# Kernel optimization log

Hardware: AMD Instinct MI355X
Metric: run time of the kernel (lower is better)

Reference implementation:

```python
import jax, jax.numpy as jnp
import numpy as np

E, T, D, H = 8, 2048, 1024, 4096
N_LAYER = 12

def setup_inputs() -> dict:
    key = jax.random.key(0)
    ks = jax.random.split(key, 4)
    x = jax.random.normal(ks[0], (E, T, D), dtype=jnp.float32)
    w_c_fc = jax.random.normal(ks[1], (E, D, H), dtype=jnp.float32) * 0.02
    w_gate = jax.random.normal(ks[2], (E, D, H), dtype=jnp.float32) * 0.02
    w_c_proj = jax.random.normal(ks[3], (E, H, D), dtype=jnp.float32) * (0.02 * (2 * N_LAYER) ** (-0.5))
    b_c_fc = jnp.zeros((E, 1, H), dtype=jnp.float32)
    b_gate = jnp.zeros((E, 1, H), dtype=jnp.float32)
    b_c_proj = jnp.zeros((E, 1, D), dtype=jnp.float32)
    return {"x": x, "w_c_fc": w_c_fc, "b_c_fc": b_c_fc, "w_gate": w_gate,
            "b_gate": b_gate, "w_c_proj": w_c_proj, "b_c_proj": b_c_proj}

def reference(x, w_c_fc, b_c_fc, w_gate, b_gate, w_c_proj, b_c_proj):
    # Per-expert SwiGLU FFN (grouped GEMM over expert dim e)
    h = jnp.einsum('eti,eih->eth', x, w_c_fc) + b_c_fc      # [E,T,H]
    g = jax.nn.silu(jnp.einsum('eti,eih->eth', x, w_gate) + b_gate)
    og = h * g                                               # gated hidden
    o = jnp.einsum('eth,eho->eto', og, w_c_proj) + b_c_proj  # [E,T,D]
    return o
```

## Files before the change

### kernel.cpp

```cpp
#include <hip/hip_runtime.h>

#define E 8
#define T 2048
#define D 1024
#define H 4096

using f32x4 = __attribute__((ext_vector_type(4))) float;
using frag8 = __attribute__((ext_vector_type(8))) short;

typedef unsigned int uint_as3 __attribute__((address_space(3)));
typedef unsigned int uint_as1 __attribute__((address_space(1)));

__device__ __forceinline__ unsigned short f2bf(float f) {
  unsigned int u = __float_as_uint(f);
  u += 0x7fffu + ((u >> 16) & 1u);
  return (unsigned short)(u >> 16);
}

__device__ __forceinline__ void gload16(const void* g, void* l) {
  __builtin_amdgcn_global_load_lds((const uint_as1*)g, (uint_as3*)l, 16, 0, 0);
}

__device__ __forceinline__ void stage8(const unsigned short* src, int ld,
                                       unsigned short* lds, int r0, int lane) {
  int lr = lane >> 3;
  int cs = lane & 7;
  int gc = cs ^ lr;
  const unsigned short* g = src + (size_t)(r0 + lr) * ld + gc * 8;
  unsigned short* l = lds + r0 * 64;
  gload16(g, l);
}

__device__ __forceinline__ frag8 read_frag(const unsigned short* lds, int row, int chunk) {
  return *(const frag8*)&lds[row * 64 + ((chunk ^ (row & 7)) << 3)];
}


__global__ __launch_bounds__(256) void convert_kernel(const float4* __restrict__ in,
                                                      ushort4* __restrict__ out, int n4) {
  int i = blockIdx.x * blockDim.x + threadIdx.x;
  int stride = gridDim.x * blockDim.x;
  for (; i < n4; i += stride) {
    float4 v = in[i];
    ushort4 o;
    o.x = f2bf(v.x); o.y = f2bf(v.y); o.z = f2bf(v.z); o.w = f2bf(v.w);
    out[i] = o;
  }
}

__global__ __launch_bounds__(256) void tconv_kernel(const float* __restrict__ in,
                                                    unsigned short* __restrict__ out,
                                                    int R, int C) {
  __shared__ float tile[32][33];
  int e = blockIdx.z;
  const float* src = in + (size_t)e * R * C;
  unsigned short* dst = out + (size_t)e * R * C;
  int c0 = blockIdx.x * 32, r0 = blockIdx.y * 32;
  int tx = threadIdx.x, ty = threadIdx.y;
#pragma unroll
  for (int i = 0; i < 32; i += 8)
    tile[ty + i][tx] = src[(size_t)(r0 + ty + i) * C + c0 + tx];
  __syncthreads();
#pragma unroll
  for (int i = 0; i < 32; i += 8)
    dst[(size_t)(c0 + ty + i) * R + r0 + tx] = f2bf(tile[tx][ty + i]);
}


__global__ __launch_bounds__(256) void gemm1_kernel(
    const unsigned short* __restrict__ xb,
    const unsigned short* __restrict__ wfcT,
    const unsigned short* __restrict__ wgT,
    const float* __restrict__ bfc,
    const float* __restrict__ bgate,
    unsigned short* __restrict__ og) {
  __shared__ unsigned short As[128 * 64];
  __shared__ unsigned short Bf[64 * 64];
  __shared__ unsigned short Bg[64 * 64];

  int bid = blockIdx.x;
  int e = bid >> 10;
  int mt = (bid >> 6) & 15;
  int nt = bid & 63;
  int m0 = mt * 128, n0 = nt * 64;

  int tid = threadIdx.x;
  int w = __builtin_amdgcn_readfirstlane(tid >> 6);
  int lane = tid & 63;

  const unsigned short* Abase = xb + (size_t)e * T * D + (size_t)m0 * D;
  const unsigned short* Fbase = wfcT + (size_t)e * H * D + (size_t)n0 * D;
  const unsigned short* Gbase = wgT + (size_t)e * H * D + (size_t)n0 * D;

  f32x4 acc_h[4][2] = {};
  f32x4 acc_g[4][2] = {};

  int wm = (w >> 1) * 64;
  int wn = (w & 1) * 32;
  int col = lane & 15, quad = lane >> 4;

  for (int k0 = 0; k0 < D; k0 += 64) {
#pragma unroll
    for (int j = 0; j < 4; ++j)
      stage8(Abase + k0, D, As, w * 32 + j * 8, lane);
#pragma unroll
    for (int j = 0; j < 2; ++j) {
      stage8(Fbase + k0, D, Bf, w * 16 + j * 8, lane);
      stage8(Gbase + k0, D, Bg, w * 16 + j * 8, lane);
    }
    __syncthreads();
#pragma unroll
    for (int kk = 0; kk < 64; kk += 32) {
      int chunk = (kk >> 3) + quad;
      frag8 a[4], fb[2], gb[2];
#pragma unroll
      for (int i = 0; i < 4; ++i)
        a[i] = read_frag(As, wm + i * 16 + col, chunk);
#pragma unroll
      for (int i = 0; i < 2; ++i) {
        fb[i] = read_frag(Bf, wn + i * 16 + col, chunk);
        gb[i] = read_frag(Bg, wn + i * 16 + col, chunk);
      }
#pragma unroll
      for (int mi = 0; mi < 4; ++mi)
#pragma unroll
        for (int ni = 0; ni < 2; ++ni) {
          acc_h[mi][ni] = __builtin_amdgcn_mfma_f32_16x16x32_bf16(a[mi], fb[ni], acc_h[mi][ni], 0, 0, 0);
          acc_g[mi][ni] = __builtin_amdgcn_mfma_f32_16x16x32_bf16(a[mi], gb[ni], acc_g[mi][ni], 0, 0, 0);
        }
    }
    __syncthreads();
  }

#pragma unroll
  for (int ni = 0; ni < 2; ++ni) {
    int n = n0 + wn + ni * 16 + col;
    float bh = bfc[e * H + n];
    float bg2 = bgate[e * H + n];
#pragma unroll
    for (int mi = 0; mi < 4; ++mi) {
#pragma unroll
      for (int i = 0; i < 4; ++i) {
        int m = m0 + wm + mi * 16 + quad * 4 + i;
        float hv = acc_h[mi][ni][i] + bh;
        float gv = acc_g[mi][ni][i] + bg2;
        float sg = gv / (1.0f + __expf(-gv));
        og[(size_t)e * T * H + (size_t)m * H + n] = f2bf(hv * sg);
      }
    }
  }
}


__global__ __launch_bounds__(256) void gemm2_kernel(
    const unsigned short* __restrict__ og,
    const unsigned short* __restrict__ wpT,
    const float* __restrict__ bproj,
    float* __restrict__ out) {
  __shared__ unsigned short As[128 * 64];
  __shared__ unsigned short Bs[128 * 64];

  int bid = blockIdx.x;
  int e = bid >> 7;
  int mt = (bid >> 3) & 15;
  int nt = bid & 7;
  int m0 = mt * 128, n0 = nt * 128;

  int tid = threadIdx.x;
  int w = __builtin_amdgcn_readfirstlane(tid >> 6);
  int lane = tid & 63;

  const unsigned short* Abase = og + (size_t)e * T * H + (size_t)m0 * H;
  const unsigned short* Bbase = wpT + (size_t)e * D * H + (size_t)n0 * H;

  f32x4 acc[4][4] = {};

  int wm = (w >> 1) * 64;
  int wn = (w & 1) * 64;
  int col = lane & 15, quad = lane >> 4;

  for (int k0 = 0; k0 < H; k0 += 64) {
#pragma unroll
    for (int j = 0; j < 4; ++j) {
      stage8(Abase + k0, H, As, w * 32 + j * 8, lane);
      stage8(Bbase + k0, H, Bs, w * 32 + j * 8, lane);
    }
    __syncthreads();
#pragma unroll
    for (int kk = 0; kk < 64; kk += 32) {
      int chunk = (kk >> 3) + quad;
      frag8 a[4], b[4];
#pragma unroll
      for (int i = 0; i < 4; ++i)
        a[i] = read_frag(As, wm + i * 16 + col, chunk);
#pragma unroll
      for (int i = 0; i < 4; ++i)
        b[i] = read_frag(Bs, wn + i * 16 + col, chunk);
#pragma unroll
      for (int mi = 0; mi < 4; ++mi)
#pragma unroll
        for (int ni = 0; ni < 4; ++ni)
          acc[mi][ni] = __builtin_amdgcn_mfma_f32_16x16x32_bf16(a[mi], b[ni], acc[mi][ni], 0, 0, 0);
    }
    __syncthreads();
  }

#pragma unroll
  for (int ni = 0; ni < 4; ++ni) {
    int n = n0 + wn + ni * 16 + col;
    float bb = bproj[e * D + n];
#pragma unroll
    for (int mi = 0; mi < 4; ++mi) {
#pragma unroll
      for (int i = 0; i < 4; ++i) {
        int m = m0 + wm + mi * 16 + quad * 4 + i;
        out[(size_t)e * T * D + (size_t)m * D + n] = acc[mi][ni][i] + bb;
      }
    }
  }
}


extern "C" void kernel_launch(void* const* d_in, const int* in_sizes, int n_in,
                              void* d_out, int out_size, void* d_ws, size_t ws_size,
                              hipStream_t stream) {
  const float* x = (const float*)d_in[0];
  const float* wfc = (const float*)d_in[1];
  const float* bfc = (const float*)d_in[2];
  const float* wg = (const float*)d_in[3];
  const float* bg = (const float*)d_in[4];
  const float* wp = (const float*)d_in[5];
  const float* bp = (const float*)d_in[6];
  float* out = (float*)d_out;

  char* ws = (char*)d_ws;
  unsigned short* xb = (unsigned short*)(ws);
  unsigned short* wfcT = (unsigned short*)(ws + 33554432);
  unsigned short* wgT = (unsigned short*)(ws + 100663296);
  unsigned short* wpT = (unsigned short*)(ws + 167772160);
  unsigned short* og = (unsigned short*)(ws + 234881024);

  convert_kernel<<<2048, 256, 0, stream>>>((const float4*)x, (ushort4*)xb,
                                           (int)((size_t)E * T * D / 4));
  tconv_kernel<<<dim3(H / 32, D / 32, E), dim3(32, 8), 0, stream>>>(wfc, wfcT, D, H);
  tconv_kernel<<<dim3(H / 32, D / 32, E), dim3(32, 8), 0, stream>>>(wg, wgT, D, H);
  tconv_kernel<<<dim3(D / 32, H / 32, E), dim3(32, 8), 0, stream>>>(wp, wpT, H, D);

  gemm1_kernel<<<E * (T / 128) * (H / 64), 256, 0, stream>>>(xb, wfcT, wgT, bfc, bg, og);
  gemm2_kernel<<<E * (T / 128) * (D / 128), 256, 0, stream>>>(og, wpT, bp, out);
}
```

Baseline: 1.038 ms.

## Triple-buffer LDS with async prefetch and larger 512-thread tiles in both GEMMs

Both GEMM kernels move to 512-thread blocks with larger output tiles (128x128 for gemm1, 256x128 for gemm2). The single-buffered load-sync-compute loop becomes a 3-stage LDS ring that prefetches tile t+2 via global_load_lds while computing tile t. Explicit vmcnt/lgkmcnt waits, raw s_barrier, sched_barrier and setprio interleave loads with MFMA bursts. The aim is to hide global memory latency and cut per-tile sync overhead, at the cost of more LDS per block (up to ~144KB in gemm1), lower occupancy, and fragile hand-counted waitcnts.

```diff
diff --git a/kernel.cpp b/kernel.cpp
--- a/kernel.cpp
+++ b/kernel.cpp
@@ -34,6 +34,9 @@
 __device__ __forceinline__ frag8 read_frag(const unsigned short* lds, int row, int chunk) {
   return *(const frag8*)&lds[row * 64 + ((chunk ^ (row & 7)) << 3)];
 }
+
+#define BARRIER() asm volatile("s_barrier" ::: "memory")
+#define WAIT_LGKM0() asm volatile("s_waitcnt lgkmcnt(0)" ::: "memory")
 
 
 __global__ __launch_bounds__(256) void convert_kernel(const float4* __restrict__ in,
@@ -67,69 +70,120 @@
 }
 
 
-__global__ __launch_bounds__(256) void gemm1_kernel(
+__global__ __launch_bounds__(512) void gemm1_kernel(
     const unsigned short* __restrict__ xb,
     const unsigned short* __restrict__ wfcT,
     const unsigned short* __restrict__ wgT,
     const float* __restrict__ bfc,
     const float* __restrict__ bgate,
     unsigned short* __restrict__ og) {
-  __shared__ unsigned short As[128 * 64];
-  __shared__ unsigned short Bf[64 * 64];
-  __shared__ unsigned short Bg[64 * 64];
+  __shared__ unsigned short As[3][128 * 64];
+  __shared__ unsigned short Bf[3][128 * 64];
+  __shared__ unsigned short Bg[3][128 * 64];
 
   int bid = blockIdx.x;
-  int e = bid >> 10;
-  int mt = (bid >> 6) & 15;
-  int nt = bid & 63;
-  int m0 = mt * 128, n0 = nt * 64;
+  int e = bid >> 9;
+  int mt = (bid >> 5) & 15;
+  int nt = bid & 31;
+  int m0 = mt * 128, n0 = nt * 128;
 
   int tid = threadIdx.x;
   int w = __builtin_amdgcn_readfirstlane(tid >> 6);
   int lane = tid & 63;
 
-  const unsigned short* Abase = xb + (size_t)e * T * D + (size_t)m0 * D;
-  const unsigned short* Fbase = wfcT + (size_t)e * H * D + (size_t)n0 * D;
-  const unsigned short* Gbase = wgT + (size_t)e * H * D + (size_t)n0 * D;
-
-  f32x4 acc_h[4][2] = {};
-  f32x4 acc_g[4][2] = {};
-
-  int wm = (w >> 1) * 64;
-  int wn = (w & 1) * 32;
+  const unsigned short* Ab = xb + (size_t)e * T * D + (size_t)m0 * D;
+  const unsigned short* Fb = wfcT + (size_t)e * H * D + (size_t)n0 * D;
+  const unsigned short* Gb = wgT + (size_t)e * H * D + (size_t)n0 * D;
+
+  f32x4 ah[4][2] = {};
+  f32x4 ag[4][2] = {};
+
+  int wm = (w >> 2) * 64;
+  int wn = (w & 3) * 32;
   int col = lane & 15, quad = lane >> 4;
-
-  for (int k0 = 0; k0 < D; k0 += 64) {
-#pragma unroll
-    for (int j = 0; j < 4; ++j)
-      stage8(Abase + k0, D, As, w * 32 + j * 8, lane);
-#pragma unroll
-    for (int j = 0; j < 2; ++j) {
-      stage8(Fbase + k0, D, Bf, w * 16 + j * 8, lane);
-      stage8(Gbase + k0, D, Bg, w * 16 + j * 8, lane);
-    }
-    __syncthreads();
-#pragma unroll
-    for (int kk = 0; kk < 64; kk += 32) {
-      int chunk = (kk >> 3) + quad;
-      frag8 a[4], fb[2], gb[2];
-#pragma unroll
-      for (int i = 0; i < 4; ++i)
-        a[i] = read_frag(As, wm + i * 16 + col, chunk);
-#pragma unroll
-      for (int i = 0; i < 2; ++i) {
-        fb[i] = read_frag(Bf, wn + i * 16 + col, chunk);
-        gb[i] = read_frag(Bg, wn + i * 16 + col, chunk);
+  int r0a = w * 8;
+
+  constexpr int NT = D / 64;
+
+#pragma unroll
+  for (int t0 = 0; t0 < 2; ++t0) {
+    stage8(Ab + t0 * 64, D, As[t0], r0a, lane);
+    stage8(Ab + t0 * 64, D, As[t0], r0a + 64, lane);
+    stage8(Fb + t0 * 64, D, Bf[t0], r0a, lane);
+    stage8(Fb + t0 * 64, D, Bf[t0], r0a + 64, lane);
+    stage8(Gb + t0 * 64, D, Bg[t0], r0a, lane);
+    stage8(Gb + t0 * 64, D, Bg[t0], r0a + 64, lane);
+  }
+  asm volatile("s_waitcnt vmcnt(6)" ::: "memory");
+  BARRIER();
+
+  int s = 0, s2 = 2;
+  for (int t = 0; t < NT; ++t) {
+    const unsigned short* Asl = As[s];
+    const unsigned short* Bfl = Bf[s];
+    const unsigned short* Bgl = Bg[s];
+    bool pf = (t + 2) < NT;
+    int kpre = (t + 2) * 64;
+
+    frag8 a[4], f[2], g[2];
+#pragma unroll
+    for (int i = 0; i < 4; ++i) a[i] = read_frag(Asl, wm + i * 16 + col, quad);
+#pragma unroll
+    for (int i = 0; i < 2; ++i) {
+      f[i] = read_frag(Bfl, wn + i * 16 + col, quad);
+      g[i] = read_frag(Bgl, wn + i * 16 + col, quad);
+    }
+    if (pf) {
+      stage8(Ab + kpre, D, As[s2], r0a, lane);
+      stage8(Ab + kpre, D, As[s2], r0a + 64, lane);
+      stage8(Fb + kpre, D, Bf[s2], r0a, lane);
+    }
+    BARRIER();
+    WAIT_LGKM0();
+    __builtin_amdgcn_sched_barrier(0);
+    __builtin_amdgcn_s_setprio(1);
+#pragma unroll
+    for (int mi = 0; mi < 4; ++mi)
+#pragma unroll
+      for (int ni = 0; ni < 2; ++ni) {
+        ah[mi][ni] = __builtin_amdgcn_mfma_f32_16x16x32_bf16(a[mi], f[ni], ah[mi][ni], 0, 0, 0);
+        ag[mi][ni] = __builtin_amdgcn_mfma_f32_16x16x32_bf16(a[mi], g[ni], ag[mi][ni], 0, 0, 0);
       }
-#pragma unroll
-      for (int mi = 0; mi < 4; ++mi)
-#pragma unroll
-        for (int ni = 0; ni < 2; ++ni) {
-          acc_h[mi][ni] = __builtin_amdgcn_mfma_f32_16x16x32_bf16(a[mi], fb[ni], acc_h[mi][ni], 0, 0, 0);
-          acc_g[mi][ni] = __builtin_amdgcn_mfma_f32_16x16x32_bf16(a[mi], gb[ni], acc_g[mi][ni], 0, 0, 0);
-        }
-    }
-    __syncthreads();
+    __builtin_amdgcn_s_setprio(0);
+    BARRIER();
+
+#pragma unroll
+    for (int i = 0; i < 4; ++i) a[i] = read_frag(Asl, wm + i * 16 + col, 4 + quad);
+#pragma unroll
+    for (int i = 0; i < 2; ++i) {
+      f[i] = read_frag(Bfl, wn + i * 16 + col, 4 + quad);
+      g[i] = read_frag(Bgl, wn + i * 16 + col, 4 + quad);
+    }
+    if (pf) {
+      stage8(Fb + kpre, D, Bf[s2], r0a + 64, lane);
+      stage8(Gb + kpre, D, Bg[s2], r0a, lane);
+      stage8(Gb + kpre, D, Bg[s2], r0a + 64, lane);
+    }
+    BARRIER();
+    WAIT_LGKM0();
+    __builtin_amdgcn_sched_barrier(0);
+    __builtin_amdgcn_s_setprio(1);
+#pragma unroll
+    for (int mi = 0; mi < 4; ++mi)
+#pragma unroll
+      for (int ni = 0; ni < 2; ++ni) {
+        ah[mi][ni] = __builtin_amdgcn_mfma_f32_16x16x32_bf16(a[mi], f[ni], ah[mi][ni], 0, 0, 0);
+        ag[mi][ni] = __builtin_amdgcn_mfma_f32_16x16x32_bf16(a[mi], g[ni], ag[mi][ni], 0, 0, 0);
+      }
+    __builtin_amdgcn_s_setprio(0);
+    if (pf)
+      asm volatile("s_waitcnt vmcnt(6)" ::: "memory");
+    else if (t + 2 == NT)
+      asm volatile("s_waitcnt vmcnt(0)" ::: "memory");
+    BARRIER();
+
+    s = (s == 2) ? 0 : s + 1;
+    s2 = (s2 == 2) ? 0 : s2 + 1;
   }
 
 #pragma unroll
@@ -142,8 +196,8 @@
 #pragma unroll
       for (int i = 0; i < 4; ++i) {
         int m = m0 + wm + mi * 16 + quad * 4 + i;
-        float hv = acc_h[mi][ni][i] + bh;
-        float gv = acc_g[mi][ni][i] + bg2;
+        float hv = ah[mi][ni][i] + bh;
+        float gv = ag[mi][ni][i] + bg2;
         float sg = gv / (1.0f + __expf(-gv));
         og[(size_t)e * T * H + (size_t)m * H + n] = f2bf(hv * sg);
       }
@@ -152,57 +206,104 @@
 }
 
 
-__global__ __launch_bounds__(256) void gemm2_kernel(
+__global__ __launch_bounds__(512) void gemm2_kernel(
     const unsigned short* __restrict__ og,
     const unsigned short* __restrict__ wpT,
     const float* __restrict__ bproj,
     float* __restrict__ out) {
-  __shared__ unsigned short As[128 * 64];
-  __shared__ unsigned short Bs[128 * 64];
+  __shared__ unsigned short As[3][256 * 64];
+  __shared__ unsigned short Bs[3][128 * 64];
 
   int bid = blockIdx.x;
-  int e = bid >> 7;
-  int mt = (bid >> 3) & 15;
+  int e = bid >> 6;
+  int mt = (bid >> 3) & 7;
   int nt = bid & 7;
-  int m0 = mt * 128, n0 = nt * 128;
+  int m0 = mt * 256, n0 = nt * 128;
 
   int tid = threadIdx.x;
   int w = __builtin_amdgcn_readfirstlane(tid >> 6);
   int lane = tid & 63;
 
-  const unsigned short* Abase = og + (size_t)e * T * H + (size_t)m0 * H;
-  const unsigned short* Bbase = wpT + (size_t)e * D * H + (size_t)n0 * H;
+  const unsigned short* Ab = og + (size_t)e * T * H + (size_t)m0 * H;
+  const unsigned short* Bb = wpT + (size_t)e * D * H + (size_t)n0 * H;
 
   f32x4 acc[4][4] = {};
 
   int wm = (w >> 1) * 64;
   int wn = (w & 1) * 64;
   int col = lane & 15, quad = lane >> 4;
-
-  for (int k0 = 0; k0 < H; k0 += 64) {
-#pragma unroll
-    for (int j = 0; j < 4; ++j) {
-      stage8(Abase + k0, H, As, w * 32 + j * 8, lane);
-      stage8(Bbase + k0, H, Bs, w * 32 + j * 8, lane);
-    }
-    __syncthreads();
-#pragma unroll
-    for (int kk = 0; kk < 64; kk += 32) {
-      int chunk = (kk >> 3) + quad;
-      frag8 a[4], b[4];
-#pragma unroll
-      for (int i = 0; i < 4; ++i)
-        a[i] = read_frag(As, wm + i * 16 + col, chunk);
-#pragma unroll
-      for (int i = 0; i < 4; ++i)
-        b[i] = read_frag(Bs, wn + i * 16 + col, chunk);
-#pragma unroll
-      for (int mi = 0; mi < 4; ++mi)
-#pragma unroll
-        for (int ni = 0; ni < 4; ++ni)
-          acc[mi][ni] = __builtin_amdgcn_mfma_f32_16x16x32_bf16(a[mi], b[ni], acc[mi][ni], 0, 0, 0);
-    }
-    __syncthreads();
+  int r0a = w * 8;
+
+  constexpr int NT = H / 64;
+
+#pragma unroll
+  for (int t0 = 0; t0 < 2; ++t0) {
+    stage8(Ab + t0 * 64, H, As[t0], r0a, lane);
+    stage8(Ab + t0 * 64, H, As[t0], r0a + 64, lane);
+    stage8(Ab + t0 * 64, H, As[t0], r0a + 128, lane);
+    stage8(Ab + t0 * 64, H, As[t0], r0a + 192, lane);
+    stage8(Bb + t0 * 64, H, Bs[t0], r0a, lane);
+    stage8(Bb + t0 * 64, H, Bs[t0], r0a + 64, lane);
+  }
+  asm volatile("s_waitcnt vmcnt(6)" ::: "memory");
+  BARRIER();
+
+  int s = 0, s2 = 2;
+  for (int t = 0; t < NT; ++t) {
+    const unsigned short* Asl = As[s];
+    const unsigned short* Bsl = Bs[s];
+    bool pf = (t + 2) < NT;
+    int kpre = (t + 2) * 64;
+
+    frag8 a[4], b[4];
+#pragma unroll
+    for (int i = 0; i < 4; ++i) a[i] = read_frag(Asl, wm + i * 16 + col, quad);
+#pragma unroll
+    for (int i = 0; i < 4; ++i) b[i] = read_frag(Bsl, wn + i * 16 + col, quad);
+    if (pf) {
+      stage8(Ab + kpre, H, As[s2], r0a, lane);
+      stage8(Ab + kpre, H, As[s2], r0a + 64, lane);
+      stage8(Bb + kpre, H, Bs[s2], r0a, lane);
+    }
+    BARRIER();
+    WAIT_LGKM0();
+    __builtin_amdgcn_sched_barrier(0);
+    __builtin_amdgcn_s_setprio(1);
+#pragma unroll
+    for (int mi = 0; mi < 4; ++mi)
+#pragma unroll
+      for (int ni = 0; ni < 4; ++ni)
+        acc[mi][ni] = __builtin_amdgcn_mfma_f32_16x16x32_bf16(a[mi], b[ni], acc[mi][ni], 0, 0, 0);
+    __builtin_amdgcn_s_setprio(0);
+    BARRIER();
+
+#pragma unroll
+    for (int i = 0; i < 4; ++i) a[i] = read_frag(Asl, wm + i * 16 + col, 4 + quad);
+#pragma unroll
+    for (int i = 0; i < 4; ++i) b[i] = read_frag(Bsl, wn + i * 16 + col, 4 + quad);
+    if (pf) {
+      stage8(Ab + kpre, H, As[s2], r0a + 128, lane);
+      stage8(Ab + kpre, H, As[s2], r0a + 192, lane);
+      stage8(Bb + kpre, H, Bs[s2], r0a + 64, lane);
+    }
+    BARRIER();
+    WAIT_LGKM0();
+    __builtin_amdgcn_sched_barrier(0);
+    __builtin_amdgcn_s_setprio(1);
+#pragma unroll
+    for (int mi = 0; mi < 4; ++mi)
+#pragma unroll
+      for (int ni = 0; ni < 4; ++ni)
+        acc[mi][ni] = __builtin_amdgcn_mfma_f32_16x16x32_bf16(a[mi], b[ni], acc[mi][ni], 0, 0, 0);
+    __builtin_amdgcn_s_setprio(0);
+    if (pf)
+      asm volatile("s_waitcnt vmcnt(6)" ::: "memory");
+    else if (t + 2 == NT)
+      asm volatile("s_waitcnt vmcnt(0)" ::: "memory");
+    BARRIER();
+
+    s = (s == 2) ? 0 : s + 1;
+    s2 = (s2 == 2) ? 0 : s2 + 1;
   }
 
 #pragma unroll
@@ -246,6 +347,6 @@
   tconv_kernel<<<dim3(H / 32, D / 32, E), dim3(32, 8), 0, stream>>>(wg, wgT, D, H);
   tconv_kernel<<<dim3(D / 32, H / 32, E), dim3(32, 8), 0, stream>>>(wp, wpT, H, D);
 
-  gemm1_kernel<<<E * (T / 128) * (H / 64), 256, 0, stream>>>(xb, wfcT, wgT, bfc, bg, og);
-  gemm2_kernel<<<E * (T / 128) * (D / 128), 256, 0, stream>>>(og, wpT, bp, out);
-}
+  gemm1_kernel<<<E * (T / 128) * (H / 128), 512, 0, stream>>>(xb, wfcT, wgT, bfc, bg, og);
+  gemm2_kernel<<<E * (T / 256) * (D / 128), 512, 0, stream>>>(og, wpT, bp, out);
+}
```

After: 1.010 ms. 1.03x faster.
